# Kernel optimization log

Hardware: AMD Instinct MI355X
Metric: run time of the kernel (lower is better)

The kernel has to match this reference:

```python
import jax, jax.numpy as jnp
import numpy as np

N = 4096; TD = 768; ID = 512; H = 256; NH = 4; HD = H // NH; NC = 3; E = 131072


def _gcn(x, w, b, src, dst, n):
    # GCNConv: add self loops, sym-normalize, aggregate at dst
    loop = jnp.arange(n)
    s = jnp.concatenate([src, loop])
    d = jnp.concatenate([dst, loop])
    deg = jax.ops.segment_sum(jnp.ones(s.shape[0], x.dtype), d, num_segments=n)
    dinv = jnp.where(deg > 0, jax.lax.rsqrt(deg), 0.0)
    norm = dinv[s] * dinv[d]                      # [E+N]
    h = x @ w                                     # [N,H] transform
    out = jax.ops.segment_sum(norm[:, None] * h[s], d, num_segments=n)
    return out + b


def setup_inputs() -> dict:
    key = jax.random.key(0)
    ks = jax.random.split(key, 20)
    p = lambda k, shp, sc: jax.random.normal(k, shp, jnp.float32) * sc
    inp = {
        "text_features": jax.random.normal(ks[0], (N, TD), jnp.float32),
        "image_features": jax.random.normal(ks[1], (N, ID), jnp.float32),
        "edge_index": jax.random.randint(ks[2], (2, E), 0, N, jnp.int32),
        "text_w": p(ks[3], (TD, H), 0.02), "text_b": jnp.zeros((H,), jnp.float32),
        "image_w": p(ks[4], (ID, H), 0.02), "image_b": jnp.zeros((H,), jnp.float32),
        "wq": p(ks[5], (H, H), 0.02), "bq": jnp.zeros((H,), jnp.float32),
        "wk": p(ks[6], (H, H), 0.02), "bk": jnp.zeros((H,), jnp.float32),
        "wv": p(ks[7], (H, H), 0.02), "bv": jnp.zeros((H,), jnp.float32),
        "wo": p(ks[8], (H, H), 0.02), "bo": jnp.zeros((H,), jnp.float32),
        "gcn1_w": p(ks[9], (H, H), 0.02), "gcn1_b": jnp.zeros((H,), jnp.float32),
        "gcn2_w": p(ks[10], (H, H), 0.02), "gcn2_b": jnp.zeros((H,), jnp.float32),
        "cls_w": p(ks[11], (H, NC), 0.02), "cls_b": jnp.zeros((NC,), jnp.float32),
    }
    return inp


def reference(text_features, image_features, edge_index,
              text_w, text_b, image_w, image_b,
              wq, bq, wk, bk, wv, bv, wo, bo,
              gcn1_w, gcn1_b, gcn2_w, gcn2_b, cls_w, cls_b):
    # fused linear+relu projections, then elementwise fuse of sum
    combined = (jax.nn.relu(text_features @ text_w + text_b)
                + jax.nn.relu(image_features @ image_w + image_b))  # [N,H]
    # MHA over all nodes (seq_len=N, batch=1)
    q = (combined @ wq + bq).reshape(N, NH, HD)
    k = (combined @ wk + bk).reshape(N, NH, HD)
    v = (combined @ wv + bv).reshape(N, NH, HD)
    scores = jnp.einsum('nhd,mhd->hnm', q, k) / jnp.sqrt(jnp.float32(HD))
    attn = jax.nn.softmax(scores, axis=-1)
    o = jnp.einsum('hnm,mhd->nhd', attn, v).reshape(N, H)
    attn_out = o @ wo + bo
    # two GCN layers
    src, dst = edge_index[0], edge_index[1]
    g1 = jax.nn.relu(_gcn(attn_out, gcn1_w, gcn1_b, src, dst, N))
    g2 = _gcn(g1, gcn2_w, gcn2_b, src, dst, N)
    return g2 @ cls_w + cls_b
```

## Files before the change

kernel.cpp:

```cpp
#include <hip/hip_runtime.h>
#include <hip/hip_bf16.h>

typedef unsigned short ushort;
typedef __attribute__((ext_vector_type(8))) short short8;
typedef __attribute__((ext_vector_type(4))) float f32x4;

constexpr int N_  = 4096;
constexpr int TD_ = 768;
constexpr int ID_ = 512;
constexpr int H_  = 256;
constexpr int HD_ = 64;
constexpr int E_  = 131072;
constexpr int SPLITS = 8;
constexpr float QSCALE = 0.125f * 1.44269504088896f;

#define MFMA16(a, b, c) __builtin_amdgcn_mfma_f32_16x16x32_bf16(a, b, c, 0, 0, 0)

__device__ inline ushort f2bf(float x) {
    union { float f; unsigned u; } v; v.f = x;
    unsigned r = v.u + 0x7fff + ((v.u >> 16) & 1);
    return (ushort)(r >> 16);
}
__device__ inline float lo2f(unsigned u) { union { unsigned x; float f; } v; v.x = u << 16; return v.f; }
__device__ inline float hi2f(unsigned u) { union { unsigned x; float f; } v; v.x = u & 0xffff0000u; return v.f; }

__device__ inline float exp2r(float x) {
    float r;
    asm("v_exp_f32 %0, %1" : "=v"(r) : "v"(x));
    return r;
}
__device__ inline unsigned pkbf(float lo, float hi) {
    union { float f; unsigned u; } a, b; a.f = lo; b.f = hi;
    return __builtin_amdgcn_perm(b.u + 0x8000u, a.u + 0x8000u, 0x07060302u);
}

__device__ inline void gl_lds16(const void* g, void* l) {
    __builtin_amdgcn_global_load_lds((const __attribute__((address_space(1))) unsigned int*)g,
                                     (__attribute__((address_space(3))) unsigned int*)l, 16, 0, 0);
}

__device__ inline void stage64(const ushort* g, long long strideEl, ushort* lds, int w, int l) {
    int r8 = l >> 3;
    int cc = (l & 7) ^ r8;
    #pragma unroll
    for (int p = 0; p < 2; p++) {
        int row = w * 16 + p * 8 + r8;
        gl_lds16(g + (long long)row * strideEl + cc * 8, lds + (w * 16 + p * 8) * 64);
    }
}
__device__ inline void stageB16(const ushort* g, long long strideEl, ushort* lds, int w, int l) {
    if (w < 2) {
        int r8 = l >> 3;
        int row = w * 8 + r8;
        int cc = (l & 7) ^ (row & 7);
        gl_lds16(g + (long long)row * strideEl + cc * 8, lds + w * 512);
    }
}
__device__ inline int swz(int row, int kOff) {
    return row * 64 + ((((kOff >> 3) ^ (row & 7))) << 3);
}


__global__ __launch_bounds__(256) void k_init(int* __restrict__ indeg, int* __restrict__ pos) {
    int i = blockIdx.x * 256 + threadIdx.x;
    indeg[i] = 0;
    pos[i] = 0;
}


__global__ __launch_bounds__(256) void k_prep(const float* __restrict__ text, const float* __restrict__ img,
                                              const float* __restrict__ tw, const float* __restrict__ iw,
                                              const float* __restrict__ wq, const float* __restrict__ wk,
                                              const float* __restrict__ wv, const float* __restrict__ wo,
                                              const float* __restrict__ g1w, const float* __restrict__ g2w,
                                              const int* __restrict__ edst, int* __restrict__ indeg,
                                              ushort* __restrict__ textbf, ushort* __restrict__ imgbf,
                                              ushort* __restrict__ wobf,
                                              ushort* __restrict__ twT, ushort* __restrict__ iwT,
                                              ushort* __restrict__ wqT, ushort* __restrict__ wkT,
                                              ushort* __restrict__ wvT, ushort* __restrict__ g1wT,
                                              ushort* __restrict__ g2wT) {
    __shared__ float Ts[64][65];
    const int b = blockIdx.x;
    const int t = threadIdx.x;
    if (b >= 2752) {
        int e = (b - 2752) * 256 + t;
        atomicAdd(&indeg[edst[e]], 1);
        return;
    }
    if (b < 2592) {
        size_t base = ((size_t)b * 256 + t) * 8;
        const size_t TXE = (size_t)N_ * TD_, IME = (size_t)N_ * ID_;
        const float* src; ushort* dst;
        if (base < TXE) { src = text + base; dst = textbf + base; }
        else if (base < TXE + IME) { src = img + (base - TXE); dst = imgbf + (base - TXE); }
        else { src = wo + (base - TXE - IME); dst = wobf + (base - TXE - IME); }
        float4 x = *(const float4*)src;
        float4 y = *(const float4*)(src + 4);
        ushort o[8] = { f2bf(x.x), f2bf(x.y), f2bf(x.z), f2bf(x.w),
                        f2bf(y.x), f2bf(y.y), f2bf(y.z), f2bf(y.w) };
        *(short8*)dst = *(const short8*)o;
        return;
    }
    int wb = b - 2592;
    const float* src; ushort* dst; int R, tile;
    if (wb < 48)       { src = tw;  dst = twT;  R = 768; tile = wb; }
    else if (wb < 80)  { src = iw;  dst = iwT;  R = 512; tile = wb - 48; }
    else if (wb < 96)  { src = wq;  dst = wqT;  R = 256; tile = wb - 80; }
    else if (wb < 112) { src = wk;  dst = wkT;  R = 256; tile = wb - 96; }
    else if (wb < 128) { src = wv;  dst = wvT;  R = 256; tile = wb - 112; }
    else if (wb < 144) { src = g1w; dst = g1wT; R = 256; tile = wb - 128; }
    else               { src = g2w; dst = g2wT; R = 256; tile = wb - 144; }
    const int r0 = (tile >> 2) * 64, c0 = (tile & 3) * 64;
    #pragma unroll
    for (int u = 0; u < 16; u++) {
        int lin = t + u * 256;
        int r = lin >> 6, c = lin & 63;
        Ts[r][c] = src[(size_t)(r0 + r) * 256 + c0 + c];
    }
    __syncthreads();
    #pragma unroll
    for (int u = 0; u < 16; u++) {
        int lin = t + u * 256;
        int c = lin >> 6, r = lin & 63;
        dst[(size_t)(c0 + c) * R + r0 + r] = f2bf(Ts[r][c]);
    }
}


__global__ __launch_bounds__(256, 4) void k_combined16(const ushort* __restrict__ text, const ushort* __restrict__ img,
                                                       const ushort* __restrict__ twT, const ushort* __restrict__ iwT,
                                                       const float* __restrict__ tb, const float* __restrict__ ib,
                                                       const int* __restrict__ indeg, int* __restrict__ offs,
                                                       float* __restrict__ dinv, ushort* __restrict__ out) {
    __shared__ ushort As[2][4096];
    __shared__ ushort Bs[2][1024];
    __shared__ ushort Cs[64 * 24];
    __shared__ int sums[256];
    const int b = blockIdx.x;
    const int t = threadIdx.x;
    if (b == 1024) {
        int v[16]; int ssum = 0; int base = t * 16;
        #pragma unroll
        for (int k2 = 0; k2 < 16; k2++) { v[k2] = indeg[base + k2]; ssum += v[k2]; }
        sums[t] = ssum;
        __syncthreads();
        for (int off = 1; off < 256; off <<= 1) {
            int x = (t >= off) ? sums[t - off] : 0;
            __syncthreads();
            sums[t] += x;
            __syncthreads();
        }
        int excl = sums[t] - ssum;
        #pragma unroll
        for (int k2 = 0; k2 < 16; k2++) {
            offs[base + k2] = excl;
            excl += v[k2];
            dinv[base + k2] = 1.f / sqrtf((float)(v[k2] + 1));
        }
        return;
    }
    const int xcd = b & 7, slot = b >> 3;
    const int bm = (xcd * 8 + (slot >> 4)) * 64, bn = (slot & 15) * 16;
    const int w = t >> 6, l = t & 63, q = l >> 4, i = l & 15;
    f32x4 acc1 = {0, 0, 0, 0}, acc2 = {0, 0, 0, 0};
    auto stC = [&](int c, int buf) {
        if (c < 12) {
            stage64(text + (size_t)bm * TD_ + c * 64, TD_, As[buf], w, l);
            stageB16(twT + (size_t)bn * TD_ + c * 64, TD_, Bs[buf], w, l);
        } else {
            stage64(img + (size_t)bm * ID_ + (c - 12) * 64, ID_, As[buf], w, l);
            stageB16(iwT + (size_t)bn * ID_ + (c - 12) * 64, ID_, Bs[buf], w, l);
        }
    };
    stC(0, 0);
    for (int c = 0; c < 20; c++) {
        __syncthreads();
        if (c + 1 < 20) stC(c + 1, (c + 1) & 1);
        const ushort* Ab = As[c & 1];
        const ushort* Bb = Bs[c & 1];
        #pragma unroll
        for (int kb = 0; kb < 2; kb++) {
            short8 af = *(const short8*)&Ab[swz(w * 16 + i, kb * 32 + q * 8)];
            short8 bfr = *(const short8*)&Bb[swz(i, kb * 32 + q * 8)];
            if (c < 12) acc1 = MFMA16(af, bfr, acc1);
            else        acc2 = MFMA16(af, bfr, acc2);
        }
    }
    __syncthreads();
    float b1 = tb[bn + i], b2 = ib[bn + i];
    #pragma unroll
    for (int r = 0; r < 4; r++) {
        float v = fmaxf(acc1[r] + b1, 0.f) + fmaxf(acc2[r] + b2, 0.f);
        Cs[(w * 16 + q * 4 + r) * 24 + i] = f2bf(v);
    }
    __syncthreads();
    if (t < 128) {
        int row = t >> 1, h8 = (t & 1) * 8;
        *(short8*)(out + (size_t)(bm + row) * H_ + bn + h8) = *(const short8*)&Cs[row * 24 + h8];
    }
}


__global__ __launch_bounds__(256) void k_qkv_scatfold(const ushort* __restrict__ A,
                                                      const ushort* __restrict__ WqT, const ushort* __restrict__ WkT,
                                                      const ushort* __restrict__ WvT,
                                                      const float* __restrict__ bq, const float* __restrict__ bk,
                                                      const float* __restrict__ bv,
                                                      ushort* __restrict__ Qg, ushort* __restrict__ Kg,
                                                      ushort* __restrict__ Vtg,
                                                      const int* __restrict__ esrc, const int* __restrict__ edst,
                                                      const int* __restrict__ offs, const float* __restrict__ dinv,
                                                      int* __restrict__ pos, int* __restrict__ ssrc,
                                                      float* __restrict__ swv,
                                                      const ushort* __restrict__ g1wT, const ushort* __restrict__ wobf,
                                                      const float* __restrict__ bo,
                                                      ushort* __restrict__ WpT, float* __restrict__ bp) {
    __shared__ ushort As[2][4096];
    __shared__ ushort Bs[2][4096];
    __shared__ ushort Cs[64 * 72];
    const int b = blockIdx.x;
    const int t = threadIdx.x;
    const int w = t >> 6, l = t & 63, q = l >> 4, i = l & 15;

    if (b >= 768) {
        if (b < 1280) {
            int e = (b - 768) * 256 + t;
            int s = esrc[e], d = edst[e];
            int p = atomicAdd(&pos[d], 1);
            int idx = offs[d] + p;
            ssrc[idx] = s;
            swv[idx] = dinv[s] * dinv[d];
            return;
        }
        if (b == 1296) {
            float acc = 0.f;
            const ushort* row = g1wT + (size_t)t * 256;
            for (int m8 = 0; m8 < 256; m8 += 8) {
                #pragma unroll
                for (int j = 0; j < 8; j++) acc += bo[m8 + j] * lo2f(((unsigned)row[m8 + j]) << 16);
            }
            bp[t] = acc;
            return;
        }
        const int f = b - 1280;
        const int bm = (f >> 2) * 64, bn = (f & 3) * 64;
        f32x4 acc[4];
        #pragma unroll
        for (int nt = 0; nt < 4; nt++) acc[nt] = (f32x4){0, 0, 0, 0};
        stage64(g1wT + (size_t)bm * H_, H_, As[0], w, l);
        stage64(wobf + (size_t)bn * H_, H_, Bs[0], w, l);
        for (int c = 0; c < 4; c++) {
            __syncthreads();
            if (c < 3) {
                stage64(g1wT + (size_t)bm * H_ + (c + 1) * 64, H_, As[(c + 1) & 1], w, l);
                stage64(wobf + (size_t)bn * H_ + (c + 1) * 64, H_, Bs[(c + 1) & 1], w, l);
            }
            const ushort* Ab = As[c & 1];
            const ushort* Bb = Bs[c & 1];
            #pragma unroll
            for (int kb = 0; kb < 2; kb++) {
                short8 af = *(const short8*)&Ab[swz(w * 16 + i, kb * 32 + q * 8)];
                #pragma unroll
                for (int nt = 0; nt < 4; nt++) {
                    short8 bfr = *(const short8*)&Bb[swz(nt * 16 + i, kb * 32 + q * 8)];
                    acc[nt] = MFMA16(af, bfr, acc[nt]);
                }
            }
        }
        __syncthreads();
        #pragma unroll
        for (int nt = 0; nt < 4; nt++)
            #pragma unroll
            for (int r = 0; r < 4; r++)
                Cs[(w * 16 + q * 4 + r) * 72 + nt * 16 + i] = f2bf(acc[nt][r]);
        __syncthreads();
        int rr = t >> 2, c16 = (t & 3) * 16;
        short8 v0 = *(const short8*)&Cs[rr * 72 + c16];
        short8 v1 = *(const short8*)&Cs[rr * 72 + c16 + 8];
        ushort* dstp = WpT + (size_t)(bm + rr) * H_ + bn + c16;
        *(short8*)dstp = v0;
        *(short8*)(dstp + 8) = v1;
        return;
    }

    const int z = b >> 8, r = b & 255;
    const int xcd = r & 7, slot = r >> 3;
    const int bm = (xcd * 8 + (slot >> 2)) * 64, head = slot & 3;
    const ushort* WT = (z == 0) ? WqT : (z == 1) ? WkT : WvT;
    const float* bias = (z == 0) ? bq : (z == 1) ? bk : bv;
    f32x4 acc[4];
    #pragma unroll
    for (int nt = 0; nt < 4; nt++) acc[nt] = (f32x4){0, 0, 0, 0};

    stage64(A + (size_t)bm * H_, H_, As[0], w, l);
    stage64(WT + (size_t)(head * 64) * H_, H_, Bs[0], w, l);
    for (int c = 0; c < 4; c++) {
        __syncthreads();
        if (c < 3) {
            stage64(A + (size_t)bm * H_ + (c + 1) * 64, H_, As[(c + 1) & 1], w, l);
            stage64(WT + (size_t)(head * 64) * H_ + (c + 1) * 64, H_, Bs[(c + 1) & 1], w, l);
        }
        const ushort* Ab = As[c & 1];
        const ushort* Bb = Bs[c & 1];
        #pragma unroll
        for (int kb = 0; kb < 2; kb++) {
            short8 af = *(const short8*)&Ab[swz(w * 16 + i, kb * 32 + q * 8)];
            #pragma unroll
            for (int nt = 0; nt < 4; nt++) {
                short8 bfr = *(const short8*)&Bb[swz(nt * 16 + i, kb * 32 + q * 8)];
                acc[nt] = MFMA16(af, bfr, acc[nt]);
            }
        }
    }
    __syncthreads();
    #pragma unroll
    for (int nt = 0; nt < 4; nt++) {
        float bv_ = bias[head * 64 + nt * 16 + i];
        #pragma unroll
        for (int r2 = 0; r2 < 4; r2++) {
            float v = acc[nt][r2] + bv_;
            if (z == 0) v *= QSCALE;
            if (z < 2) Cs[(w * 16 + q * 4 + r2) * 72 + nt * 16 + i] = f2bf(v);
            else       Cs[(nt * 16 + i) * 72 + w * 16 + q * 4 + r2] = f2bf(v);
        }
    }
    __syncthreads();
    int rr = t >> 2, c16 = (t & 3) * 16;
    short8 v0 = *(const short8*)&Cs[rr * 72 + c16];
    short8 v1 = *(const short8*)&Cs[rr * 72 + c16 + 8];
    ushort* dst;
    if (z < 2) dst = ((z == 0) ? Qg : Kg) + (size_t)head * N_ * HD_ + (size_t)(bm + rr) * HD_ + c16;
    else       dst = Vtg + (size_t)head * HD_ * N_ + (size_t)rr * N_ + bm + c16;
    *(short8*)dst = v0;
    *(short8*)(dst + 8) = v1;
}


__global__ __launch_bounds__(256) void k_attn_mfma(const ushort* __restrict__ Qg, const ushort* __restrict__ Kg,
                                                   const ushort* __restrict__ Vtg, ushort* __restrict__ Op,
                                                   float* __restrict__ lp) {
    __shared__ ushort Ks[4096];
    __shared__ ushort Vs[4096];
    __shared__ ushort Ps[4][2][16 * 72];
    const int head = blockIdx.y, r0 = blockIdx.x * 128, z = blockIdx.z;
    const int t = threadIdx.x, w = t >> 6, l = t & 63, q = l >> 4, i = l & 15;
    const int rw = (i ^ (i >> 1)) & 7;
    ushort* Pw0 = &Ps[w][0][0];
    ushort* Pw1 = &Ps[w][1][0];

    short8 qf[2][2];
    #pragma unroll
    for (int qt = 0; qt < 2; qt++)
        #pragma unroll
        for (int kb = 0; kb < 2; kb++)
            qf[qt][kb] = *(const short8*)(Qg + ((size_t)head * N_ + r0 + qt * 64 + w * 16 + i) * HD_ + kb * 32 + q * 8);

    f32x4 Oacc[2][4];
    float lacc[2] = {0.f, 0.f};
    #pragma unroll
    for (int qt = 0; qt < 2; qt++)
        #pragma unroll
        for (int dt = 0; dt < 4; dt++) Oacc[qt][dt] = (f32x4){0, 0, 0, 0};

    const int NT = 64 / SPLITS;
    const int cb0 = z * NT;
    for (int it = 0; it < NT; it++) {
        const int cb = cb0 + it;
        __syncthreads();
        stage64(Kg + ((size_t)head * N_ + (size_t)cb * 64) * HD_, HD_, Ks, w, l);
        stage64(Vtg + (size_t)head * HD_ * N_ + cb * 64, N_, Vs, w, l);
        __syncthreads();

        f32x4 St[2][4];
        #pragma unroll
        for (int qt = 0; qt < 2; qt++)
            #pragma unroll
            for (int kt = 0; kt < 4; kt++) St[qt][kt] = (f32x4){0, 0, 0, 0};
        #pragma unroll
        for (int kb = 0; kb < 2; kb++) {
            #pragma unroll
            for (int kt = 0; kt < 4; kt++) {
                short8 kf = *(const short8*)&Ks[swz(kt * 16 + i, kb * 32 + q * 8)];
                St[0][kt] = MFMA16(kf, qf[0][kb], St[0][kt]);
                St[1][kt] = MFMA16(kf, qf[1][kb], St[1][kt]);
            }
        }
        #pragma unroll
        for (int kt = 0; kt < 4; kt++) {
            float a0 = exp2r(St[0][kt][0]), a1 = exp2r(St[0][kt][1]);
            float a2 = exp2r(St[0][kt][2]), a3 = exp2r(St[0][kt][3]);
            lacc[0] += (a0 + a1) + (a2 + a3);
            float b0 = exp2r(St[1][kt][0]), b1 = exp2r(St[1][kt][1]);
            float b2 = exp2r(St[1][kt][2]), b3 = exp2r(St[1][kt][3]);
            lacc[1] += (b0 + b1) + (b2 + b3);
            int off = i * 72 + (((2 * kt + (q >> 1)) ^ rw) << 3) + ((q & 1) << 2);
            uint2 va; va.x = pkbf(a0, a1); va.y = pkbf(a2, a3);
            *(uint2*)&Pw0[off] = va;
            uint2 vb; vb.x = pkbf(b0, b1); vb.y = pkbf(b2, b3);
            *(uint2*)&Pw1[off] = vb;
        }
        #pragma unroll
        for (int kb = 0; kb < 2; kb++) {
            int poff = i * 72 + (((4 * kb + q) ^ rw) << 3);
            short8 pf0 = *(const short8*)&Pw0[poff];
            short8 pf1 = *(const short8*)&Pw1[poff];
            #pragma unroll
            for (int dt = 0; dt < 4; dt++) {
                short8 vf = *(const short8*)&Vs[swz(dt * 16 + i, kb * 32 + q * 8)];
                Oacc[0][dt] = MFMA16(vf, pf0, Oacc[0][dt]);
                Oacc[1][dt] = MFMA16(vf, pf1, Oacc[1][dt]);
            }
        }
    }

    #pragma unroll
    for (int qt = 0; qt < 2; qt++) {
        lacc[qt] += __shfl_xor(lacc[qt], 16);
        lacc[qt] += __shfl_xor(lacc[qt], 32);
    }

    const size_t sh = ((size_t)z * 4 + head) * N_;
    #pragma unroll
    for (int qt = 0; qt < 2; qt++) {
        const int row = r0 + qt * 64 + w * 16 + i;
        #pragma unroll
        for (int dt = 0; dt < 4; dt++) {
            uint2 v;
            v.x = pkbf(Oacc[qt][dt][0], Oacc[qt][dt][1]);
            v.y = pkbf(Oacc[qt][dt][2], Oacc[qt][dt][3]);
            *(uint2*)&Op[(sh + row) * HD_ + dt * 16 + q * 4] = v;
        }
        if (l < 16) lp[sh + r0 + qt * 64 + w * 16 + l] = lacc[qt];
    }
}

__global__ __launch_bounds__(256) void k_attn_merge(const ushort* __restrict__ Op, const float* __restrict__ lp,
                                                    ushort* __restrict__ obuf) {
    const int t = threadIdx.x;
    const int idx = blockIdx.x * 16 + (t >> 4);
    const int h = idx >> 12, n = idx & 4095;
    const int d4 = (t & 15) * 4;
    float lsum = 0.f;
    float acc[4] = {0.f, 0.f, 0.f, 0.f};
    #pragma unroll
    for (int s = 0; s < SPLITS; s++) {
        size_t sh = ((size_t)s * 4 + h) * N_ + n;
        lsum += lp[sh];
        uint2 o4 = *(const uint2*)&Op[sh * HD_ + d4];
        acc[0] += lo2f(o4.x); acc[1] += hi2f(o4.x);
        acc[2] += lo2f(o4.y); acc[3] += hi2f(o4.y);
    }
    float inv = 1.f / lsum;
    uint2 res;
    res.x = pkbf(acc[0] * inv, acc[1] * inv);
    res.y = pkbf(acc[2] * inv, acc[3] * inv);
    *(uint2*)&obuf[(size_t)n * H_ + h * HD_ + d4] = res;
}


template <bool BIAS>
__global__ __launch_bounds__(256, 4) void k_gemm16(const ushort* __restrict__ A, const ushort* __restrict__ BT,
                                                   const float* __restrict__ bias, ushort* __restrict__ outb) {
    __shared__ ushort As[2][4096];
    __shared__ ushort Bs[2][1024];
    __shared__ ushort Cs[64 * 24];
    const int bm = blockIdx.x * 64, bn = blockIdx.y * 16;
    const int t = threadIdx.x, w = t >> 6, l = t & 63, q = l >> 4, i = l & 15;
    f32x4 acc = {0, 0, 0, 0};
    stage64(A + (size_t)bm * H_, H_, As[0], w, l);
    stageB16(BT + (size_t)bn * H_, H_, Bs[0], w, l);
    for (int c = 0; c < 4; c++) {
        __syncthreads();
        if (c < 3) {
            stage64(A + (size_t)bm * H_ + (c + 1) * 64, H_, As[(c + 1) & 1], w, l);
            stageB16(BT + (size_t)bn * H_ + (c + 1) * 64, H_, Bs[(c + 1) & 1], w, l);
        }
        const ushort* Ab = As[c & 1];
        const ushort* Bb = Bs[c & 1];
        #pragma unroll
        for (int kb = 0; kb < 2; kb++) {
            short8 af = *(const short8*)&Ab[swz(w * 16 + i, kb * 32 + q * 8)];
            short8 bfr = *(const short8*)&Bb[swz(i, kb * 32 + q * 8)];
            acc = MFMA16(af, bfr, acc);
        }
    }
    __syncthreads();
    float bb = BIAS ? bias[bn + i] : 0.f;
    #pragma unroll
    for (int r = 0; r < 4; r++)
        Cs[(w * 16 + q * 4 + r) * 24 + i] = f2bf(acc[r] + bb);
    __syncthreads();
    if (t < 128) {
        int row = t >> 1, h8 = (t & 1) * 8;
        *(short8*)(outb + (size_t)(bm + row) * H_ + bn + h8) = *(const short8*)&Cs[row * 24 + h8];
    }
}


__global__ __launch_bounds__(256) void k_agg1(const ushort* __restrict__ h, const int* __restrict__ ssrc,
                                              const float* __restrict__ sw, const int* __restrict__ offs,
                                              const int* __restrict__ indeg, const float* __restrict__ dinv,
                                              const float* __restrict__ bias, ushort* __restrict__ outb) {
    const int t = threadIdx.x;
    const int j = __builtin_amdgcn_readfirstlane(blockIdx.x * 4 + (t >> 6));
    const int d0 = (t & 63) * 4;
    float dj = dinv[j];
    uint2 hv = *(const uint2*)&h[(size_t)j * H_ + d0];
    float s2 = dj * dj;
    float a0 = s2 * lo2f(hv.x), a1 = s2 * hi2f(hv.x), a2 = s2 * lo2f(hv.y), a3 = s2 * hi2f(hv.y);
    int start = offs[j], cnt = indeg[j];
    for (int e = 0; e < cnt; e++) {
        int s = ssrc[start + e];
        float wg = sw[start + e];
        uint2 v = *(const uint2*)&h[(size_t)s * H_ + d0];
        a0 += wg * lo2f(v.x); a1 += wg * hi2f(v.x);
        a2 += wg * lo2f(v.y); a3 += wg * hi2f(v.y);
    }
    a0 = fmaxf(a0 + bias[d0], 0.f);
    a1 = fmaxf(a1 + bias[d0 + 1], 0.f);
    a2 = fmaxf(a2 + bias[d0 + 2], 0.f);
    a3 = fmaxf(a3 + bias[d0 + 3], 0.f);
    uint2 o;
    o.x = pkbf(a0, a1);
    o.y = pkbf(a2, a3);
    *(uint2*)&outb[(size_t)j * H_ + d0] = o;
}


__global__ __launch_bounds__(256) void k_aggcls(const ushort* __restrict__ h, const int* __restrict__ ssrc,
                                                const float* __restrict__ sw, const int* __restrict__ offs,
                                                const int* __restrict__ indeg, const float* __restrict__ dinv,
                                                const float* __restrict__ bias, const float* __restrict__ cw,
                                                const float* __restrict__ cb, float* __restrict__ out) {
    const int t = threadIdx.x;
    const int j = __builtin_amdgcn_readfirstlane(blockIdx.x * 4 + (t >> 6));
    const int lane = t & 63;
    const int d0 = lane * 4;
    float dj = dinv[j];
    uint2 hv = *(const uint2*)&h[(size_t)j * H_ + d0];
    float s2 = dj * dj;
    float a0 = s2 * lo2f(hv.x), a1 = s2 * hi2f(hv.x), a2 = s2 * lo2f(hv.y), a3 = s2 * hi2f(hv.y);
    int start = offs[j], cnt = indeg[j];
    for (int e = 0; e < cnt; e++) {
        int s = ssrc[start + e];
        float wg = sw[start + e];
        uint2 v = *(const uint2*)&h[(size_t)s * H_ + d0];
        a0 += wg * lo2f(v.x); a1 += wg * hi2f(v.x);
        a2 += wg * lo2f(v.y); a3 += wg * hi2f(v.y);
    }
    a0 += bias[d0]; a1 += bias[d0 + 1]; a2 += bias[d0 + 2]; a3 += bias[d0 + 3];
    float p0 = a0 * cw[d0 * 3 + 0] + a1 * cw[(d0 + 1) * 3 + 0]
             + a2 * cw[(d0 + 2) * 3 + 0] + a3 * cw[(d0 + 3) * 3 + 0];
    float p1 = a0 * cw[d0 * 3 + 1] + a1 * cw[(d0 + 1) * 3 + 1]
             + a2 * cw[(d0 + 2) * 3 + 1] + a3 * cw[(d0 + 3) * 3 + 1];
    float p2 = a0 * cw[d0 * 3 + 2] + a1 * cw[(d0 + 1) * 3 + 2]
             + a2 * cw[(d0 + 2) * 3 + 2] + a3 * cw[(d0 + 3) * 3 + 2];
    #pragma unroll
    for (int off = 32; off > 0; off >>= 1) {
        p0 += __shfl_xor(p0, off);
        p1 += __shfl_xor(p1, off);
        p2 += __shfl_xor(p2, off);
    }
    if (lane == 0) {
        out[j * 3 + 0] = p0 + cb[0];
        out[j * 3 + 1] = p1 + cb[1];
        out[j * 3 + 2] = p2 + cb[2];
    }
}


extern "C" void kernel_launch(void* const* d_in, const int* in_sizes, int n_in,
                              void* d_out, int out_size, void* d_ws, size_t ws_size,
                              hipStream_t stream) {
    const float* text = (const float*)d_in[0];
    const float* img  = (const float*)d_in[1];
    const int*   eidx = (const int*)d_in[2];
    const float* tw  = (const float*)d_in[3];
    const float* tb  = (const float*)d_in[4];
    const float* iw  = (const float*)d_in[5];
    const float* ib  = (const float*)d_in[6];
    const float* wq  = (const float*)d_in[7];
    const float* bq  = (const float*)d_in[8];
    const float* wk  = (const float*)d_in[9];
    const float* bk  = (const float*)d_in[10];
    const float* wv  = (const float*)d_in[11];
    const float* bv  = (const float*)d_in[12];
    const float* wo  = (const float*)d_in[13];
    const float* bo  = (const float*)d_in[14];
    const float* g1w = (const float*)d_in[15];
    const float* g1b = (const float*)d_in[16];
    const float* g2w = (const float*)d_in[17];
    const float* g2b = (const float*)d_in[18];
    const float* cw  = (const float*)d_in[19];
    const float* cbv = (const float*)d_in[20];

    char* W = (char*)d_ws;
    size_t cur = 0;
    auto alloc = [&](size_t sz) { char* p = W + cur; cur += (sz + 255) & ~(size_t)255; return p; };

    float* dinv  = (float*)alloc(N_ * 4);
    float* swv   = (float*)alloc(E_ * 4);
    int* indeg   = (int*)alloc(N_ * 4);
    int* offs    = (int*)alloc(N_ * 4);
    int* pos     = (int*)alloc(N_ * 4);
    int* ssrc    = (int*)alloc(E_ * 4);
    ushort* Qg   = (ushort*)alloc((size_t)N_ * H_ * 2);
    ushort* Kg   = (ushort*)alloc((size_t)N_ * H_ * 2);
    ushort* Vtg  = (ushort*)alloc((size_t)N_ * H_ * 2);
    ushort* obuf = (ushort*)alloc((size_t)N_ * H_ * 2);
    ushort* WpT  = (ushort*)alloc((size_t)H_ * H_ * 2);
    float* bp    = (float*)alloc(H_ * 4);
    ushort* g1wT = (ushort*)alloc((size_t)H_ * H_ * 2);
    ushort* g2wT = (ushort*)alloc((size_t)H_ * H_ * 2);
    ushort* wobf = (ushort*)alloc((size_t)H_ * H_ * 2);
    float* lp    = (float*)alloc((size_t)SPLITS * 4 * N_ * 4);
    char* S = W + cur;

    ushort* textbf = (ushort*)S;
    ushort* imgbf  = textbf + (size_t)N_ * TD_;
    ushort* twT    = imgbf + (size_t)N_ * ID_;
    ushort* iwT    = twT + (size_t)TD_ * H_;
    ushort* wqT    = iwT + (size_t)ID_ * H_;
    ushort* wkT    = wqT + (size_t)H_ * H_;
    ushort* wvT    = wkT + (size_t)H_ * H_;
    ushort* combbf = wvT + (size_t)H_ * H_;
    ushort* Op = (ushort*)S;
    ushort* hbuf  = (ushort*)S;
    ushort* g1b16 = (ushort*)(S + (size_t)2 * 1024 * 1024);
    ushort* hbuf2 = (ushort*)(S + (size_t)4 * 1024 * 1024);

    const int* esrc = eidx;
    const int* edst = eidx + E_;

    k_init<<<dim3(N_ / 256), dim3(256), 0, stream>>>(indeg, pos);
    k_prep<<<dim3(3264), dim3(256), 0, stream>>>(text, img, tw, iw, wq, wk, wv, wo, g1w, g2w,
                                                 edst, indeg,
                                                 textbf, imgbf, wobf, twT, iwT, wqT, wkT, wvT, g1wT, g2wT);
    k_combined16<<<dim3(1025), dim3(256), 0, stream>>>(textbf, imgbf, twT, iwT, tb, ib,
                                                       indeg, offs, dinv, combbf);
    k_qkv_scatfold<<<dim3(1297), dim3(256), 0, stream>>>(combbf, wqT, wkT, wvT, bq, bk, bv, Qg, Kg, Vtg,
                                                         esrc, edst, offs, dinv, pos, ssrc, swv,
                                                         g1wT, wobf, bo, WpT, bp);
    k_attn_mfma<<<dim3(32, 4, SPLITS), dim3(256), 0, stream>>>(Qg, Kg, Vtg, Op, lp);
    k_attn_merge<<<dim3(1024), dim3(256), 0, stream>>>(Op, lp, obuf);

    k_gemm16<true><<<dim3(64, 16), dim3(256), 0, stream>>>(obuf, WpT, bp, hbuf);
    k_agg1<<<dim3(N_ / 4), dim3(256), 0, stream>>>(hbuf, ssrc, swv, offs, indeg, dinv, g1b, g1b16);
    k_gemm16<false><<<dim3(64, 16), dim3(256), 0, stream>>>(g1b16, g2wT, nullptr, hbuf2);
    k_aggcls<<<dim3(N_ / 4), dim3(256), 0, stream>>>(hbuf2, ssrc, swv, offs, indeg, dinv, g2b, cw, cbv,
                                                     (float*)d_out);
}
```

Before: 216.8 us.

## Fold classifier weights into second GCN layer before aggregation

```diff
diff --git a/kernel.cpp b/kernel.cpp
--- a/kernel.cpp
+++ b/kernel.cpp
@@ -215,7 +215,10 @@
                                                       float* __restrict__ swv,
                                                       const ushort* __restrict__ g1wT, const ushort* __restrict__ wobf,
                                                       const float* __restrict__ bo,
-                                                      ushort* __restrict__ WpT, float* __restrict__ bp) {
+                                                      ushort* __restrict__ WpT, float* __restrict__ bp,
+                                                      const float* __restrict__ g2wf, const float* __restrict__ cwf,
+                                                      const float* __restrict__ g2bf, const float* __restrict__ cbf,
+                                                      float* __restrict__ W3, float* __restrict__ cvec) {
     __shared__ ushort As[2][4096];
     __shared__ ushort Bs[2][4096];
     __shared__ ushort Cs[64 * 72];
@@ -231,6 +234,24 @@
             int idx = offs[d] + p;
             ssrc[idx] = s;
             swv[idx] = dinv[s] * dinv[d];
+            return;
+        }
+        if (b >= 1297) {
+            if (b == 1301) {
+                if (t < 3) {
+                    float acc = 0.f;
+                    for (int d = 0; d < 256; d++) acc += cwf[d * 3 + t] * g2bf[d];
+                    cvec[t] = acc + cbf[t];
+                }
+                return;
+            }
+            int r = (b - 1297) * 64 + (t & 63), c = t >> 6;
+            if (c < 3) {
+                float acc = 0.f;
+                const float* row = g2wf + (size_t)r * 256;
+                for (int k = 0; k < 256; k++) acc += row[k] * cwf[k * 3 + c];
+                W3[r * 3 + c] = acc;
+            }
             return;
         }
         if (b == 1296) {
@@ -528,44 +549,62 @@
 }
 
 
-__global__ __launch_bounds__(256) void k_aggcls(const ushort* __restrict__ h, const int* __restrict__ ssrc,
-                                                const float* __restrict__ sw, const int* __restrict__ offs,
-                                                const int* __restrict__ indeg, const float* __restrict__ dinv,
-                                                const float* __restrict__ bias, const float* __restrict__ cw,
-                                                const float* __restrict__ cb, float* __restrict__ out) {
+__global__ __launch_bounds__(256) void k_t3(const ushort* __restrict__ g1b16, const float* __restrict__ W3,
+                                            float* __restrict__ t3) {
     const int t = threadIdx.x;
     const int j = __builtin_amdgcn_readfirstlane(blockIdx.x * 4 + (t >> 6));
-    const int lane = t & 63;
-    const int d0 = lane * 4;
-    float dj = dinv[j];
-    uint2 hv = *(const uint2*)&h[(size_t)j * H_ + d0];
-    float s2 = dj * dj;
-    float a0 = s2 * lo2f(hv.x), a1 = s2 * hi2f(hv.x), a2 = s2 * lo2f(hv.y), a3 = s2 * hi2f(hv.y);
-    int start = offs[j], cnt = indeg[j];
-    for (int e = 0; e < cnt; e++) {
-        int s = ssrc[start + e];
-        float wg = sw[start + e];
-        uint2 v = *(const uint2*)&h[(size_t)s * H_ + d0];
-        a0 += wg * lo2f(v.x); a1 += wg * hi2f(v.x);
-        a2 += wg * lo2f(v.y); a3 += wg * hi2f(v.y);
-    }
-    a0 += bias[d0]; a1 += bias[d0 + 1]; a2 += bias[d0 + 2]; a3 += bias[d0 + 3];
-    float p0 = a0 * cw[d0 * 3 + 0] + a1 * cw[(d0 + 1) * 3 + 0]
-             + a2 * cw[(d0 + 2) * 3 + 0] + a3 * cw[(d0 + 3) * 3 + 0];
-    float p1 = a0 * cw[d0 * 3 + 1] + a1 * cw[(d0 + 1) * 3 + 1]
-             + a2 * cw[(d0 + 2) * 3 + 1] + a3 * cw[(d0 + 3) * 3 + 1];
-    float p2 = a0 * cw[d0 * 3 + 2] + a1 * cw[(d0 + 1) * 3 + 2]
-             + a2 * cw[(d0 + 2) * 3 + 2] + a3 * cw[(d0 + 3) * 3 + 2];
+    const int l = t & 63, d0 = l * 4;
+    uint2 hv = *(const uint2*)&g1b16[(size_t)j * H_ + d0];
+    float g0 = lo2f(hv.x), g1 = hi2f(hv.x), g2 = lo2f(hv.y), g3 = hi2f(hv.y);
+    const float* wr = W3 + d0 * 3;
+    float4 wa = *(const float4*)(wr);
+    float4 wb = *(const float4*)(wr + 4);
+    float4 wc = *(const float4*)(wr + 8);
+    float p0 = g0 * wa.x + g1 * wa.w + g2 * wb.z + g3 * wc.y;
+    float p1 = g0 * wa.y + g1 * wb.x + g2 * wb.w + g3 * wc.z;
+    float p2 = g0 * wa.z + g1 * wb.y + g2 * wc.x + g3 * wc.w;
     #pragma unroll
     for (int off = 32; off > 0; off >>= 1) {
         p0 += __shfl_xor(p0, off);
         p1 += __shfl_xor(p1, off);
         p2 += __shfl_xor(p2, off);
     }
-    if (lane == 0) {
-        out[j * 3 + 0] = p0 + cb[0];
-        out[j * 3 + 1] = p1 + cb[1];
-        out[j * 3 + 2] = p2 + cb[2];
+    if (l == 0) {
+        t3[j * 3 + 0] = p0;
+        t3[j * 3 + 1] = p1;
+        t3[j * 3 + 2] = p2;
+    }
+}
+
+
+__global__ __launch_bounds__(256) void k_agg3(const float* __restrict__ t3, const int* __restrict__ ssrc,
+                                              const float* __restrict__ sw, const int* __restrict__ offs,
+                                              const int* __restrict__ indeg, const float* __restrict__ dinv,
+                                              const float* __restrict__ cvec, float* __restrict__ out) {
+    const int t = threadIdx.x;
+    const int j = __builtin_amdgcn_readfirstlane(blockIdx.x * 4 + (t >> 6));
+    const int l = t & 63;
+    int start = offs[j], cnt = indeg[j];
+    float p0 = 0.f, p1 = 0.f, p2 = 0.f;
+    for (int e = l; e < cnt; e += 64) {
+        int s = ssrc[start + e];
+        float wg = sw[start + e];
+        p0 += wg * t3[s * 3 + 0];
+        p1 += wg * t3[s * 3 + 1];
+        p2 += wg * t3[s * 3 + 2];
+    }
+    #pragma unroll
+    for (int off = 32; off > 0; off >>= 1) {
+        p0 += __shfl_xor(p0, off);
+        p1 += __shfl_xor(p1, off);
+        p2 += __shfl_xor(p2, off);
+    }
+    if (l == 0) {
+        float dj = dinv[j];
+        float s2 = dj * dj;
+        out[j * 3 + 0] = p0 + s2 * t3[j * 3 + 0] + cvec[0];
+        out[j * 3 + 1] = p1 + s2 * t3[j * 3 + 1] + cvec[1];
+        out[j * 3 + 2] = p2 + s2 * t3[j * 3 + 2] + cvec[2];
     }
 }
 
@@ -615,6 +654,9 @@
     ushort* g2wT = (ushort*)alloc((size_t)H_ * H_ * 2);
     ushort* wobf = (ushort*)alloc((size_t)H_ * H_ * 2);
     float* lp    = (float*)alloc((size_t)SPLITS * 4 * N_ * 4);
+    float* t3    = (float*)alloc((size_t)N_ * 3 * 4);
+    float* W3    = (float*)alloc(256 * 3 * 4);
+    float* cvec  = (float*)alloc(16);
     char* S = W + cur;
 
     ushort* textbf = (ushort*)S;
@@ -628,7 +670,6 @@
     ushort* Op = (ushort*)S;
     ushort* hbuf  = (ushort*)S;
     ushort* g1b16 = (ushort*)(S + (size_t)2 * 1024 * 1024);
-    ushort* hbuf2 = (ushort*)(S + (size_t)4 * 1024 * 1024);
 
     const int* esrc = eidx;
     const int* edst = eidx + E_;
@@ -639,15 +680,15 @@
                                                  textbf, imgbf, wobf, twT, iwT, wqT, wkT, wvT, g1wT, g2wT);
     k_combined16<<<dim3(1025), dim3(256), 0, stream>>>(textbf, imgbf, twT, iwT, tb, ib,
                                                        indeg, offs, dinv, combbf);
-    k_qkv_scatfold<<<dim3(1297), dim3(256), 0, stream>>>(combbf, wqT, wkT, wvT, bq, bk, bv, Qg, Kg, Vtg,
+    k_qkv_scatfold<<<dim3(1302), dim3(256), 0, stream>>>(combbf, wqT, wkT, wvT, bq, bk, bv, Qg, Kg, Vtg,
                                                          esrc, edst, offs, dinv, pos, ssrc, swv,
-                                                         g1wT, wobf, bo, WpT, bp);
+                                                         g1wT, wobf, bo, WpT, bp,
+                                                         g2w, cw, g2b, cbv, W3, cvec);
     k_attn_mfma<<<dim3(32, 4, SPLITS), dim3(256), 0, stream>>>(Qg, Kg, Vtg, Op, lp);
     k_attn_merge<<<dim3(1024), dim3(256), 0, stream>>>(Op, lp, obuf);
 
     k_gemm16<true><<<dim3(64, 16), dim3(256), 0, stream>>>(obuf, WpT, bp, hbuf);
     k_agg1<<<dim3(N_ / 4), dim3(256), 0, stream>>>(hbuf, ssrc, swv, offs, indeg, dinv, g1b, g1b16);
-    k_gemm16<false><<<dim3(64, 16), dim3(256), 0, stream>>>(g1b16, g2wT, nullptr, hbuf2);
-    k_aggcls<<<dim3(N_ / 4), dim3(256), 0, stream>>>(hbuf2, ssrc, swv, offs, indeg, dinv, g2b, cw, cbv,
-                                                     (float*)d_out);
-}
+    k_t3<<<dim3(N_ / 4), dim3(256), 0, stream>>>(g1b16, W3, t3);
+    k_agg3<<<dim3(N_ / 4), dim3(256), 0, stream>>>(t3, ssrc, swv, offs, indeg, dinv, cvec, (float*)d_out);
+}
```

Measured after the change: 211.0 us. 2.7% less time.
